# Performance work log

Hardware: AMD Instinct MI355X
Metric: run time of the kernel (lower is better)

Reference implementation:

```python
import jax, jax.numpy as jnp
import numpy as np

B, C, L = 8, 256, 2048


def setup_inputs() -> dict:
    key = jax.random.key(0)
    ks = jax.random.split(key, 7)
    s = 0.05
    return {
        "x": jax.random.normal(ks[0], (B, C, L), dtype=jnp.float32),
        "Wq": jax.random.normal(ks[1], (C, C), dtype=jnp.float32) * s,
        "bq": jax.random.normal(ks[2], (C,), dtype=jnp.float32) * s,
        "Wk": jax.random.normal(ks[3], (C, C), dtype=jnp.float32) * s,
        "bk": jax.random.normal(ks[4], (C,), dtype=jnp.float32) * s,
        "Wv": jax.random.normal(ks[5], (C, C), dtype=jnp.float32) * s,
        "bv": jax.random.normal(ks[6], (C,), dtype=jnp.float32) * s,
    }


def reference(x, Wq, bq, Wk, bk, Wv, bv):
    # Conv1d with kernel_size=1 == per-position linear over channels.
    # x: [B, C, L]
    scale = x.shape[1] ** (-0.5)
    q = jnp.einsum('oc,bcl->bol', Wq, x) + bq[None, :, None]  # [B,C,L]
    k = jnp.einsum('oc,bcl->bol', Wk, x) + bk[None, :, None]
    v = jnp.einsum('oc,bcl->bol', Wv, x) + bv[None, :, None]
    scores = jnp.einsum('bcl,bcm->blm', q, k) * scale          # [B,L,L]
    attn = jax.nn.softmax(scores, axis=-1)
    context = jnp.einsum('blm,bcm->bcl', attn, v)              # [B,C,L]
    return context + x
```

## Files before the change

### kernel.cpp

```cpp
#include <hip/hip_runtime.h>

#define NB 8
#define NC 256
#define NL 2048
#define SCALE 0.0625f

typedef __attribute__((ext_vector_type(8))) __bf16 bf16x8;
typedef __attribute__((ext_vector_type(4))) float f32x4;
typedef __attribute__((ext_vector_type(4))) unsigned int u32x4;
typedef __attribute__((ext_vector_type(4))) unsigned short u16x4;
typedef __attribute__((ext_vector_type(8))) unsigned short u16x8;

static __device__ __forceinline__ unsigned short f2b(float f) {
    unsigned int u = __builtin_bit_cast(unsigned int, f);
    u += 0x7fffu + ((u >> 16) & 1u);
    return (unsigned short)(u >> 16);
}

__global__ void wconv_kernel(const float* __restrict__ Wq,
                             const float* __restrict__ Wk,
                             const float* __restrict__ Wv,
                             unsigned short* __restrict__ Wbf)
{
    const int base = (blockIdx.x * 256 + threadIdx.x) * 4;
    const int mat  = base >> 16;
    const int off  = base & 65535;
    const float* W = (mat == 0) ? Wq : (mat == 1) ? Wk : Wv;
    float4 w = *(const float4*)&W[off];
    u16x4 p = {f2b(w.x), f2b(w.y), f2b(w.z), f2b(w.w)};
    *(u16x4*)&Wbf[base] = p;
}

__global__ __launch_bounds__(256, 2) void xprep_kernel(
    const float* __restrict__ x, unsigned short* __restrict__ xT)
{
    const int b  = blockIdx.z;
    const int c0 = blockIdx.y * 64;
    const int l0 = blockIdx.x * 64;
    const int t  = threadIdx.x;

    __shared__ unsigned short Tr[64][68];

    #pragma unroll
    for (int p = 0; p < 4; ++p) {
        const int c  = p * 16 + (t >> 4);
        const int lg = t & 15;
        float4 xv = *(const float4*)&x[((size_t)(b * NC + c0 + c)) * NL + l0 + lg * 4];
        u16x4 pk = {f2b(xv.x), f2b(xv.y), f2b(xv.z), f2b(xv.w)};
        *(u16x4*)&Tr[c][lg * 4] = pk;
    }
    __syncthreads();
    #pragma unroll
    for (int j = 0; j < 2; ++j) {
        const int chunk = t + 256 * j;
        const int l  = chunk >> 3;
        const int ck = chunk & 7;
        u16x8 o;
        #pragma unroll
        for (int i = 0; i < 8; ++i) o[i] = Tr[ck * 8 + i][l];
        *(u16x8*)&xT[((size_t)(b * NL + l0 + l)) * NC + c0 + ck * 8] = o;
    }
}

__global__ __launch_bounds__(256, 2) void qkv_mfma(
    const unsigned short* __restrict__ xT,
    const unsigned short* __restrict__ Wbf,
    const float* __restrict__ bq, const float* __restrict__ bk,
    const float* __restrict__ bv,
    unsigned short* __restrict__ qT, unsigned short* __restrict__ kT,
    unsigned short* __restrict__ vo)
{
    const int raw = blockIdx.x;
    const int b   = raw & 7;
    const int rem = raw >> 3;
    const int mat = rem >> 5;
    const int lt0 = (rem & 31) * 64;
    const int t    = threadIdx.x;
    const int w    = t >> 6;
    const int lane = t & 63;
    const int ln15 = lane & 15;
    const int quad = lane >> 4;

    __shared__ __align__(16) unsigned short XT[64 * 256];
    __shared__ __align__(16) unsigned short WC[256 * 64];

    const unsigned short* Wm = Wbf + mat * 65536;
    const float* bias = (mat == 0) ? bq : (mat == 1) ? bk : bv;

    float bvals[4][4];
    #pragma unroll
    for (int ot = 0; ot < 4; ++ot)
        #pragma unroll
        for (int r = 0; r < 4; ++r)
            bvals[ot][r] = bias[w * 64 + ot * 16 + quad * 4 + r];

    #pragma unroll
    for (int s = 0; s < 8; ++s) {
        const int il = w * 8 + s;
        const int n  = il * 2 + (lane >> 5);
        const int p  = lane & 31;
        const int g  = p ^ (n & 15);
        const unsigned short* gp = &xT[((size_t)(b * NL + lt0 + n)) * NC + g * 8];
        __builtin_amdgcn_global_load_lds(
            (const __attribute__((address_space(1))) unsigned int*)gp,
            (__attribute__((address_space(3))) unsigned int*)&XT[il * 512],
            16, 0, 0);
    }

    f32x4 acc[4][4];
    #pragma unroll
    for (int i = 0; i < 4; ++i)
        #pragma unroll
        for (int j = 0; j < 4; ++j) acc[i][j] = f32x4{0.f, 0.f, 0.f, 0.f};

    for (int k0 = 0; k0 < 4; ++k0) {
        if (k0) __syncthreads();
        #pragma unroll
        for (int s = 0; s < 8; ++s) {
            const int il = w * 8 + s;
            const int o  = il * 8 + (lane >> 3);
            const int p  = lane & 7;
            const int g  = p ^ (o & 7);
            const unsigned short* gp = &Wm[(size_t)o * NC + k0 * 64 + g * 8];
            __builtin_amdgcn_global_load_lds(
                (const __attribute__((address_space(1))) unsigned int*)gp,
                (__attribute__((address_space(3))) unsigned int*)&WC[il * 512],
                16, 0, 0);
        }
        __syncthreads();

        #pragma unroll
        for (int ks = 0; ks < 2; ++ks) {
            bf16x8 xf[4];
            #pragma unroll
            for (int lt = 0; lt < 4; ++lt) {
                const int l  = lt * 16 + ln15;
                const int kc = k0 * 8 + ks * 4 + quad;
                const int pp = kc ^ (l & 15);
                xf[lt] = __builtin_bit_cast(bf16x8, *(const u32x4*)&XT[l * 256 + pp * 8]);
            }
            #pragma unroll
            for (int ot = 0; ot < 4; ++ot) {
                const int o  = w * 64 + ot * 16 + ln15;
                const int pp = (ks * 4 + quad) ^ (o & 7);
                bf16x8 wf = __builtin_bit_cast(bf16x8, *(const u32x4*)&WC[o * 64 + pp * 8]);
                #pragma unroll
                for (int lt = 0; lt < 4; ++lt)
                    acc[ot][lt] = __builtin_amdgcn_mfma_f32_16x16x32_bf16(
                                      wf, xf[lt], acc[ot][lt], 0, 0, 0);
            }
        }
    }

    if (mat < 2) {
        unsigned short* out = (mat == 0) ? qT : kT;
        #pragma unroll
        for (int ot = 0; ot < 4; ++ot) {
            const int o_base = w * 64 + ot * 16 + quad * 4;
            #pragma unroll
            for (int lt = 0; lt < 4; ++lt) {
                const int l = lt0 + lt * 16 + ln15;
                u16x4 pk;
                #pragma unroll
                for (int r = 0; r < 4; ++r)
                    pk[r] = f2b(acc[ot][lt][r] + bvals[ot][r]);
                *(u16x4*)&out[((size_t)(b * NL + l)) * NC + o_base] = pk;
            }
        }
    } else {
        #pragma unroll
        for (int ot = 0; ot < 4; ++ot)
            #pragma unroll
            for (int lt = 0; lt < 4; ++lt) {
                const int l = lt0 + lt * 16 + ln15;
                #pragma unroll
                for (int r = 0; r < 4; ++r) {
                    const int o = w * 64 + ot * 16 + quad * 4 + r;
                    vo[((size_t)(b * NC + o)) * NL + l] = f2b(acc[ot][lt][r] + bvals[ot][r]);
                }
            }
    }
}

__global__ __launch_bounds__(256, 2) void attn_kernel(
    const unsigned short* __restrict__ qT,
    const unsigned short* __restrict__ kT,
    const unsigned short* __restrict__ v,
    const float* __restrict__ x,
    float* __restrict__ out)
{
    const int raw  = blockIdx.x;
    const int b    = raw & 7;
    const int l0   = (raw >> 3) * 64;
    const int t    = threadIdx.x;
    const int w    = t >> 6;
    const int lane = t & 63;
    const int ln15 = lane & 15;
    const int quad = lane >> 4;

    __shared__ __align__(16) char smem[73984];
    unsigned short* Klds = (unsigned short*)smem;
    unsigned short* Vlds = (unsigned short*)(smem + 32768);
    unsigned short* Plds = (unsigned short*)(smem + 65536);
    float*          denom = (float*)(smem + 73728);
    float (*T)[68] = (float(*)[68])smem;

    bf16x8 qf[8];
    {
        const size_t qrow = ((size_t)b * NL + l0 + w * 16 + ln15) * NC;
        #pragma unroll
        for (int kt = 0; kt < 8; ++kt)
            qf[kt] = __builtin_bit_cast(bf16x8,
                        *(const u32x4*)&qT[qrow + kt * 32 + quad * 8]);
    }
    if (t < 64) denom[t] = 0.0f;

    f32x4 ctx[16];
    #pragma unroll
    for (int i = 0; i < 16; ++i) ctx[i] = f32x4{0.f, 0.f, 0.f, 0.f};

    for (int mt = 0; mt < 32; ++mt) {
        const int m0 = mt * 64;
        __syncthreads();

        #pragma unroll
        for (int s = 0; s < 8; ++s) {
            const int il = w * 8 + s;
            const int n  = il * 2 + (lane >> 5);
            const int p  = lane & 31;
            const int g  = p ^ (n & 15);
            const unsigned short* gp = &kT[((size_t)b * NL + m0 + n) * NC + g * 8];
            __builtin_amdgcn_global_load_lds(
                (const __attribute__((address_space(1))) unsigned int*)gp,
                (__attribute__((address_space(3))) unsigned int*)&Klds[il * 512],
                16, 0, 0);
        }
        #pragma unroll
        for (int s = 0; s < 8; ++s) {
            const int il = w * 8 + s;
            const int c  = il * 8 + (lane >> 3);
            const int p  = lane & 7;
            const int g  = p ^ (c & 7);
            const unsigned short* gp = &v[((size_t)(b * NC + c)) * NL + m0 + g * 8];
            __builtin_amdgcn_global_load_lds(
                (const __attribute__((address_space(1))) unsigned int*)gp,
                (__attribute__((address_space(3))) unsigned int*)&Vlds[il * 512],
                16, 0, 0);
        }
        __syncthreads();

        f32x4 sacc[4];
        #pragma unroll
        for (int nt = 0; nt < 4; ++nt) sacc[nt] = f32x4{0.f, 0.f, 0.f, 0.f};
        #pragma unroll
        for (int nt = 0; nt < 4; ++nt) {
            const int n = nt * 16 + ln15;
            #pragma unroll
            for (int kt = 0; kt < 8; ++kt) {
                const int p = (kt * 4 + quad) ^ ln15;
                bf16x8 bf = __builtin_bit_cast(bf16x8,
                              *(const u32x4*)&Klds[n * 256 + p * 8]);
                sacc[nt] = __builtin_amdgcn_mfma_f32_16x16x32_bf16(
                               qf[kt], bf, sacc[nt], 0, 0, 0);
            }
        }

        float rs[4] = {0.f, 0.f, 0.f, 0.f};
        #pragma unroll
        for (int nt = 0; nt < 4; ++nt) {
            #pragma unroll
            for (int r = 0; r < 4; ++r) {
                float e = __expf(sacc[nt][r] * SCALE);
                rs[r] += e;
                const int ip = w * 16 + quad * 4 + r;
                const int j  = nt * 16 + ln15;
                const int pc = (j >> 3) ^ (ip & 7);
                Plds[ip * 64 + pc * 8 + (j & 7)] = f2b(e);
            }
        }
        #pragma unroll
        for (int r = 0; r < 4; ++r) {
            rs[r] += __shfl_xor(rs[r], 1, 64);
            rs[r] += __shfl_xor(rs[r], 2, 64);
            rs[r] += __shfl_xor(rs[r], 4, 64);
            rs[r] += __shfl_xor(rs[r], 8, 64);
        }
        if (ln15 == 0) {
            #pragma unroll
            for (int r = 0; r < 4; ++r) denom[w * 16 + quad * 4 + r] += rs[r];
        }

        bf16x8 pf[2];
        {
            const int m = w * 16 + ln15;
            #pragma unroll
            for (int kt = 0; kt < 2; ++kt) {
                const int p = (kt * 4 + quad) ^ (m & 7);
                pf[kt] = __builtin_bit_cast(bf16x8,
                           *(const u32x4*)&Plds[m * 64 + p * 8]);
            }
        }
        #pragma unroll
        for (int ct = 0; ct < 16; ++ct) {
            const int c = ct * 16 + ln15;
            #pragma unroll
            for (int kt = 0; kt < 2; ++kt) {
                const int p = (kt * 4 + quad) ^ (c & 7);
                bf16x8 vb = __builtin_bit_cast(bf16x8,
                              *(const u32x4*)&Vlds[c * 64 + p * 8]);
                ctx[ct] = __builtin_amdgcn_mfma_f32_16x16x32_bf16(
                              pf[kt], vb, ctx[ct], 0, 0, 0);
            }
        }
    }

    __syncthreads();
    float dinv[4];
    #pragma unroll
    for (int r = 0; r < 4; ++r) dinv[r] = 1.0f / denom[w * 16 + quad * 4 + r];

    const int col  = t & 63;
    const int colg = t >> 6;
    for (int gq = 0; gq < 4; ++gq) {
        __syncthreads();
        #pragma unroll
        for (int ctl = 0; ctl < 4; ++ctl) {
            const int ct = gq * 4 + ctl;
            f32x4 val;
            #pragma unroll
            for (int r = 0; r < 4; ++r) val[r] = ctx[ct][r] * dinv[r];
            *(f32x4*)&T[ctl * 16 + ln15][w * 16 + quad * 4] = val;
        }
        __syncthreads();
        #pragma unroll
        for (int rr = 0; rr < 16; ++rr) {
            const int cl = colg * 16 + rr;
            const size_t idx = ((size_t)(b * NC + gq * 64 + cl)) * NL + l0 + col;
            out[idx] = T[cl][col] + x[idx];
        }
    }
}

extern "C" void kernel_launch(void* const* d_in, const int* in_sizes, int n_in,
                              void* d_out, int out_size, void* d_ws, size_t ws_size,
                              hipStream_t stream) {
    const float* x  = (const float*)d_in[0];
    const float* Wq = (const float*)d_in[1];
    const float* bq = (const float*)d_in[2];
    const float* Wk = (const float*)d_in[3];
    const float* bk = (const float*)d_in[4];
    const float* Wv = (const float*)d_in[5];
    const float* bv = (const float*)d_in[6];
    float* out = (float*)d_out;

    const size_t plane = (size_t)NB * NC * NL;
    unsigned short* qT  = (unsigned short*)d_ws;
    unsigned short* kT  = qT + plane;
    unsigned short* v   = kT + plane;
    unsigned short* xT  = v + plane;
    unsigned short* Wbf = xT + plane;

    wconv_kernel<<<192, 256, 0, stream>>>(Wq, Wk, Wv, Wbf);

    dim3 gx(NL / 64, NC / 64, NB);
    xprep_kernel<<<gx, 256, 0, stream>>>(x, xT);

    qkv_mfma<<<768, 256, 0, stream>>>(xT, Wbf, bq, bk, bv, qT, kT, v);

    attn_kernel<<<256, 256, 0, stream>>>(qT, kT, v, x, out);
}
```

Baseline: 180.5 us.

## Double-buffer K/V tiles and split key dimension across two warp groups in attention

The attention kernel now runs 512 threads per block. Warps are split into four query groups and two key-half groups, and each key-half group computes half of the 64-key tile's scores and its own partial PV accumulation. K/V tiles are double-buffered in LDS, so the next tile's global->LDS load is issued before computing on the current one, with one barrier per iteration instead of two. The partial contexts and denominators are reduced through LDS at the end, and the epilogue writes with float4 vectorised loads and stores. The cost is roughly 137KB of LDS and one block per CU, which lowers occupancy.

```diff
diff --git a/kernel.cpp b/kernel.cpp
--- a/kernel.cpp
+++ b/kernel.cpp
@@ -182,7 +182,7 @@
     }
 }
 
-__global__ __launch_bounds__(256, 2) void attn_kernel(
+__global__ __launch_bounds__(512, 1) void attn_kernel(
     const unsigned short* __restrict__ qT,
     const unsigned short* __restrict__ kT,
     const unsigned short* __restrict__ v,
@@ -197,69 +197,80 @@
     const int lane = t & 63;
     const int ln15 = lane & 15;
     const int quad = lane >> 4;
-
-    __shared__ __align__(16) char smem[73984];
-    unsigned short* Klds = (unsigned short*)smem;
-    unsigned short* Vlds = (unsigned short*)(smem + 32768);
-    unsigned short* Plds = (unsigned short*)(smem + 65536);
-    float*          denom = (float*)(smem + 73728);
-    float (*T)[68] = (float(*)[68])smem;
+    const int qg   = w & 3;
+    const int kg   = w >> 2;
+
+    __shared__ __align__(16) char smem[139776];
+    unsigned short* Kb0 = (unsigned short*)smem;
+    unsigned short* Kb1 = (unsigned short*)(smem + 32768);
+    unsigned short* Vb0 = (unsigned short*)(smem + 65536);
+    unsigned short* Vb1 = (unsigned short*)(smem + 98304);
+    unsigned short* Plds = (unsigned short*)(smem + 131072);
+    float* denomP = (float*)(smem + 139264);
+    float (*ctxbuf)[68] = (float(*)[68])smem;
 
     bf16x8 qf[8];
     {
-        const size_t qrow = ((size_t)b * NL + l0 + w * 16 + ln15) * NC;
+        const size_t qrow = ((size_t)b * NL + l0 + qg * 16 + ln15) * NC;
         #pragma unroll
         for (int kt = 0; kt < 8; ++kt)
             qf[kt] = __builtin_bit_cast(bf16x8,
                         *(const u32x4*)&qT[qrow + kt * 32 + quad * 8]);
     }
-    if (t < 64) denom[t] = 0.0f;
 
     f32x4 ctx[16];
     #pragma unroll
     for (int i = 0; i < 16; ++i) ctx[i] = f32x4{0.f, 0.f, 0.f, 0.f};
-
-    for (int mt = 0; mt < 32; ++mt) {
+    float dacc[4] = {0.f, 0.f, 0.f, 0.f};
+
+    auto stage = [&](int mt, unsigned short* Kd, unsigned short* Vd) {
         const int m0 = mt * 64;
-        __syncthreads();
-
-        #pragma unroll
-        for (int s = 0; s < 8; ++s) {
-            const int il = w * 8 + s;
+        #pragma unroll
+        for (int s = 0; s < 4; ++s) {
+            const int il = w * 4 + s;
             const int n  = il * 2 + (lane >> 5);
-            const int p  = lane & 31;
-            const int g  = p ^ (n & 15);
+            const int g  = (lane & 31) ^ (n & 15);
             const unsigned short* gp = &kT[((size_t)b * NL + m0 + n) * NC + g * 8];
             __builtin_amdgcn_global_load_lds(
                 (const __attribute__((address_space(1))) unsigned int*)gp,
-                (__attribute__((address_space(3))) unsigned int*)&Klds[il * 512],
+                (__attribute__((address_space(3))) unsigned int*)&Kd[il * 512],
                 16, 0, 0);
         }
         #pragma unroll
-        for (int s = 0; s < 8; ++s) {
-            const int il = w * 8 + s;
+        for (int s = 0; s < 4; ++s) {
+            const int il = w * 4 + s;
             const int c  = il * 8 + (lane >> 3);
-            const int p  = lane & 7;
-            const int g  = p ^ (c & 7);
+            const int g  = (lane & 7) ^ (c & 7);
             const unsigned short* gp = &v[((size_t)(b * NC + c)) * NL + m0 + g * 8];
             __builtin_amdgcn_global_load_lds(
                 (const __attribute__((address_space(1))) unsigned int*)gp,
-                (__attribute__((address_space(3))) unsigned int*)&Vlds[il * 512],
+                (__attribute__((address_space(3))) unsigned int*)&Vd[il * 512],
                 16, 0, 0);
         }
-        __syncthreads();
-
-        f32x4 sacc[4];
-        #pragma unroll
-        for (int nt = 0; nt < 4; ++nt) sacc[nt] = f32x4{0.f, 0.f, 0.f, 0.f};
-        #pragma unroll
-        for (int nt = 0; nt < 4; ++nt) {
-            const int n = nt * 16 + ln15;
+    };
+
+    stage(0, Kb0, Vb0);
+    __syncthreads();
+
+    for (int mt = 0; mt < 32; ++mt) {
+        if (mt < 31) {
+            if (mt & 1) stage(mt + 1, Kb0, Vb0);
+            else        stage(mt + 1, Kb1, Vb1);
+        }
+        const unsigned short* Kd = (mt & 1) ? Kb1 : Kb0;
+        const unsigned short* Vd = (mt & 1) ? Vb1 : Vb0;
+
+        f32x4 sacc[2];
+        sacc[0] = f32x4{0.f, 0.f, 0.f, 0.f};
+        sacc[1] = f32x4{0.f, 0.f, 0.f, 0.f};
+        #pragma unroll
+        for (int nt = 0; nt < 2; ++nt) {
+            const int n = kg * 32 + nt * 16 + ln15;
             #pragma unroll
             for (int kt = 0; kt < 8; ++kt) {
                 const int p = (kt * 4 + quad) ^ ln15;
                 bf16x8 bf = __builtin_bit_cast(bf16x8,
-                              *(const u32x4*)&Klds[n * 256 + p * 8]);
+                              *(const u32x4*)&Kd[n * 256 + p * 8]);
                 sacc[nt] = __builtin_amdgcn_mfma_f32_16x16x32_bf16(
                                qf[kt], bf, sacc[nt], 0, 0, 0);
             }
@@ -267,13 +278,13 @@
 
         float rs[4] = {0.f, 0.f, 0.f, 0.f};
         #pragma unroll
-        for (int nt = 0; nt < 4; ++nt) {
+        for (int nt = 0; nt < 2; ++nt) {
             #pragma unroll
             for (int r = 0; r < 4; ++r) {
                 float e = __expf(sacc[nt][r] * SCALE);
                 rs[r] += e;
-                const int ip = w * 16 + quad * 4 + r;
-                const int j  = nt * 16 + ln15;
+                const int ip = qg * 16 + quad * 4 + r;
+                const int j  = kg * 32 + nt * 16 + ln15;
                 const int pc = (j >> 3) ^ (ip & 7);
                 Plds[ip * 64 + pc * 8 + (j & 7)] = f2b(e);
             }
@@ -284,60 +295,72 @@
             rs[r] += __shfl_xor(rs[r], 2, 64);
             rs[r] += __shfl_xor(rs[r], 4, 64);
             rs[r] += __shfl_xor(rs[r], 8, 64);
-        }
-        if (ln15 == 0) {
-            #pragma unroll
-            for (int r = 0; r < 4; ++r) denom[w * 16 + quad * 4 + r] += rs[r];
-        }
-
-        bf16x8 pf[2];
+            dacc[r] += rs[r];
+        }
+
+        bf16x8 pf;
         {
-            const int m = w * 16 + ln15;
-            #pragma unroll
-            for (int kt = 0; kt < 2; ++kt) {
-                const int p = (kt * 4 + quad) ^ (m & 7);
-                pf[kt] = __builtin_bit_cast(bf16x8,
-                           *(const u32x4*)&Plds[m * 64 + p * 8]);
-            }
+            const int m = qg * 16 + ln15;
+            const int p = (kg * 4 + quad) ^ (m & 7);
+            pf = __builtin_bit_cast(bf16x8, *(const u32x4*)&Plds[m * 64 + p * 8]);
         }
         #pragma unroll
         for (int ct = 0; ct < 16; ++ct) {
             const int c = ct * 16 + ln15;
-            #pragma unroll
-            for (int kt = 0; kt < 2; ++kt) {
-                const int p = (kt * 4 + quad) ^ (c & 7);
-                bf16x8 vb = __builtin_bit_cast(bf16x8,
-                              *(const u32x4*)&Vlds[c * 64 + p * 8]);
-                ctx[ct] = __builtin_amdgcn_mfma_f32_16x16x32_bf16(
-                              pf[kt], vb, ctx[ct], 0, 0, 0);
-            }
-        }
-    }
-
+            const int p = (kg * 4 + quad) ^ (c & 7);
+            bf16x8 vb = __builtin_bit_cast(bf16x8,
+                          *(const u32x4*)&Vd[c * 64 + p * 8]);
+            ctx[ct] = __builtin_amdgcn_mfma_f32_16x16x32_bf16(
+                          pf, vb, ctx[ct], 0, 0, 0);
+        }
+
+        __syncthreads();
+    }
+
+    if (kg == 1) {
+        #pragma unroll
+        for (int ct = 0; ct < 16; ++ct) {
+            const int c = ct * 16 + ln15;
+            #pragma unroll
+            for (int r = 0; r < 4; ++r)
+                ctxbuf[c][qg * 16 + quad * 4 + r] = ctx[ct][r];
+        }
+    }
+    if (ln15 == 0) {
+        #pragma unroll
+        for (int r = 0; r < 4; ++r)
+            denomP[kg * 64 + qg * 16 + quad * 4 + r] = dacc[r];
+    }
     __syncthreads();
-    float dinv[4];
-    #pragma unroll
-    for (int r = 0; r < 4; ++r) dinv[r] = 1.0f / denom[w * 16 + quad * 4 + r];
-
-    const int col  = t & 63;
-    const int colg = t >> 6;
-    for (int gq = 0; gq < 4; ++gq) {
-        __syncthreads();
-        #pragma unroll
-        for (int ctl = 0; ctl < 4; ++ctl) {
-            const int ct = gq * 4 + ctl;
-            f32x4 val;
-            #pragma unroll
-            for (int r = 0; r < 4; ++r) val[r] = ctx[ct][r] * dinv[r];
-            *(f32x4*)&T[ctl * 16 + ln15][w * 16 + quad * 4] = val;
-        }
-        __syncthreads();
-        #pragma unroll
-        for (int rr = 0; rr < 16; ++rr) {
-            const int cl = colg * 16 + rr;
-            const size_t idx = ((size_t)(b * NC + gq * 64 + cl)) * NL + l0 + col;
-            out[idx] = T[cl][col] + x[idx];
-        }
+    if (kg == 0) {
+        float rinv[4];
+        #pragma unroll
+        for (int r = 0; r < 4; ++r) {
+            const int ql = qg * 16 + quad * 4 + r;
+            rinv[r] = 1.0f / (denomP[ql] + denomP[64 + ql]);
+        }
+        #pragma unroll
+        for (int ct = 0; ct < 16; ++ct) {
+            const int c = ct * 16 + ln15;
+            #pragma unroll
+            for (int r = 0; r < 4; ++r) {
+                const int ql = qg * 16 + quad * 4 + r;
+                ctxbuf[c][ql] = (ctx[ct][r] + ctxbuf[c][ql]) * rinv[r];
+            }
+        }
+    }
+    __syncthreads();
+
+    #pragma unroll
+    for (int p = 0; p < 8; ++p) {
+        const int f  = t + 512 * p;
+        const int c  = f >> 4;
+        const int lg = (f & 15) * 4;
+        const size_t idx = ((size_t)(b * NC + c)) * NL + l0 + lg;
+        float4 xv = *(const float4*)&x[idx];
+        float4 cv = *(const float4*)&ctxbuf[c][lg];
+        float4 o = make_float4(cv.x + xv.x, cv.y + xv.y, cv.z + xv.z, cv.w + xv.w);
+        *(float4*)&out[idx] = o;
     }
 }
 
@@ -367,5 +390,5 @@
 
     qkv_mfma<<<768, 256, 0, stream>>>(xT, Wbf, bq, bk, bv, qT, kT, v);
 
-    attn_kernel<<<256, 256, 0, stream>>>(qT, kT, v, x, out);
-}
+    attn_kernel<<<256, 512, 0, stream>>>(qT, kT, v, x, out);
+}
```

Measured after the change: 165.3 us. 1.09x faster.
